# Optimization experiments

Measured on AMD Instinct MI355X. Metric: run time of the kernel, lower is better.

Reference implementation:

```python
import jax, jax.numpy as jnp
import numpy as np

B, T_ENC, IN, H, SEQ_OUT = 1024, 50, 99, 2112, 25


def _lstm_cell(x, h, c, W_ih, b_ih, W_hh, b_hh):
    # gates: [B, 4H], torch LSTMCell gate order is i, f, g, o
    gates = x @ W_ih.T + b_ih + h @ W_hh.T + b_hh
    i, f, g, o = jnp.split(gates, 4, axis=-1)
    c_new = jax.nn.sigmoid(f) * c + jax.nn.sigmoid(i) * jnp.tanh(g)
    h_new = jax.nn.sigmoid(o) * jnp.tanh(c_new)
    return h_new, c_new


def setup_inputs() -> dict:
    key = jax.random.key(0)
    ks = jax.random.split(key, 14)
    s = 0.04
    return {
        "hidden_states": jax.random.normal(ks[0], (B, T_ENC, H), jnp.float32),
        "cell_states": jax.random.normal(ks[1], (B, T_ENC, H), jnp.float32),
        "global_t_state": jax.random.normal(ks[2], (B, H), jnp.float32),
        "p": jax.random.normal(ks[3], (B, 1, IN), jnp.float32),
        "W_ih0": jax.random.normal(ks[4], (4 * H, IN), jnp.float32) * s,
        "b_ih0": jax.random.normal(ks[5], (4 * H,), jnp.float32) * s,
        "W_hh0": jax.random.normal(ks[6], (4 * H, H), jnp.float32) * s,
        "b_hh0": jax.random.normal(ks[7], (4 * H,), jnp.float32) * s,
        "W_ih1": jax.random.normal(ks[8], (4 * H, H), jnp.float32) * s,
        "b_ih1": jax.random.normal(ks[9], (4 * H,), jnp.float32) * s,
        "W_hh1": jax.random.normal(ks[10], (4 * H, H), jnp.float32) * s,
        "b_hh1": jax.random.normal(ks[11], (4 * H,), jnp.float32) * s,
        "W_out": jax.random.normal(ks[12], (H, IN), jnp.float32) * s,
        "b_out": jax.random.normal(ks[13], (IN,), jnp.float32) * s,
    }


def reference(hidden_states, cell_states, global_t_state, p,
              W_ih0, b_ih0, W_hh0, b_hh0,
              W_ih1, b_ih1, W_hh1, b_hh1,
              W_out, b_out):
    # initial states: layer 0 uses mean over encoder hidden states,
    # layer 1 uses mean over [global_t_state ; hidden_states]
    h0 = hidden_states.mean(axis=1)                                   # [B, H]
    h1 = jnp.concatenate((global_t_state[:, None, :], hidden_states), axis=1).mean(axis=1)
    c0 = cell_states.mean(axis=1)
    c1 = c0
    pre0 = p[:, 0, :]                                                 # seed input [B, IN]

    def step(carry, _):
        h0, c0, h1, c1, prev = carry
        h0n, c0n = _lstm_cell(prev, h0, c0, W_ih0, b_ih0, W_hh0, b_hh0)
        h1n, c1n = _lstm_cell(h0n, h1, c1, W_ih1, b_ih1, W_hh1, b_hh1)
        pre = h1n @ W_out + b_out + prev                              # residual on cell-0 input
        return (h0n, c0n, h1n, c1n, pre), pre

    _, pres = jax.lax.scan(step, (h0, c0, h1, c1, pre0), None, length=SEQ_OUT)
    return pres.transpose(1, 0, 2)                                    # [B, SEQ_OUT, IN]
```

## Files before the change

### kernel.cpp

```cpp
#include <hip/hip_runtime.h>

#define B_    1024
#define H_    2112
#define FH    8448
#define IN_   99
#define TENC  50
#define SEQ   25
#define K0    2240
#define K1    4224
#define LDX0  2240
#define LDX1  4224

typedef __bf16 bf16;
typedef __bf16 bf16x8 __attribute__((ext_vector_type(8)));
typedef __bf16 bf16x4 __attribute__((ext_vector_type(4)));
typedef float  f32x4  __attribute__((ext_vector_type(4)));

__device__ __forceinline__ void gload_lds16(const void* g, void* l) {
  __builtin_amdgcn_global_load_lds(
      (const __attribute__((address_space(1))) void*)g,
      (__attribute__((address_space(3))) void*)l, 16, 0, 0);
}

__device__ __forceinline__ float sigf(float x) { return 1.f / (1.f + __expf(-x)); }
__device__ __forceinline__ float tanhfast(float x) { return 1.f - 2.f / (__expf(2.f * x) + 1.f); }

__global__ __launch_bounds__(256, 2)
void lstm_gemm_cell(const bf16* __restrict__ X, int lda, int K,
                    const bf16* __restrict__ W,
                    const float* __restrict__ bsum,
                    float* __restrict__ Cst,
                    bf16* __restrict__ d1, int ld1,
                    bf16* __restrict__ d2, int ld2)
{
  __shared__ __align__(16) bf16 As0[128 * 32];
  __shared__ __align__(16) bf16 As1[128 * 32];
  __shared__ __align__(16) bf16 Bs0[128 * 32];
  __shared__ __align__(16) bf16 Bs1[128 * 32];

  const int vid = (blockIdx.x & 7) * 66 + (blockIdx.x >> 3);
  const int hb  = vid >> 3;
  const int hc0 = hb * 32;
  const int m0  = (vid & 7) * 128;

  const int tid  = threadIdx.x;
  const int srow = tid >> 2;
  const int scol = (tid & 3) * 8;

  const bf16* Ab = X + (size_t)(m0 + srow) * lda + scol;
  const bf16* Bb = W + ((size_t)((srow >> 5) * H_ + hc0 + (srow & 31))) * K + scol;
  const size_t HK2 = (size_t)2 * H_ * K;

  const int lane = tid & 63;
  const int wv = tid >> 6;
  const int wm = wv >> 1, wn = wv & 1;
  const int lr = lane & 15, lq = lane >> 4;

  f32x4 acc[4][4];
#pragma unroll
  for (int a = 0; a < 4; ++a)
#pragma unroll
    for (int b = 0; b < 4; ++b) acc[a][b] = (f32x4){0.f, 0.f, 0.f, 0.f};

#define STAGE(kt, AD, BD) do {                                              \
    const int ko_ = (kt) * 32;                                              \
    gload_lds16(Ab + (size_t)0 * lda + ko_,  &AD[0 * 2048 + tid * 8]);      \
    gload_lds16(Ab + (size_t)64 * lda + ko_, &AD[1 * 2048 + tid * 8]);      \
    gload_lds16(Bb + ko_,                    &BD[0 * 2048 + tid * 8]);      \
    gload_lds16(Bb + HK2 + ko_,              &BD[1 * 2048 + tid * 8]);      \
  } while (0)

#define COMPUTE(AS, BS) do {                                                \
    bf16x8 af_[4], bf_[4];                                                  \
    _Pragma("unroll")                                                       \
    for (int mi = 0; mi < 4; ++mi)                                          \
      af_[mi] = *(const bf16x8*)&AS[(wm * 64 + mi * 16 + lr) * 32 + lq * 8];\
    _Pragma("unroll")                                                       \
    for (int nf = 0; nf < 4; ++nf)                                          \
      bf_[nf] = *(const bf16x8*)&BS[(nf * 32 + wn * 16 + lr) * 32 + lq * 8];\
    _Pragma("unroll")                                                       \
    for (int mi = 0; mi < 4; ++mi)                                          \
      _Pragma("unroll")                                                     \
      for (int nf = 0; nf < 4; ++nf)                                        \
        acc[mi][nf] = __builtin_amdgcn_mfma_f32_16x16x32_bf16(              \
            af_[mi], bf_[nf], acc[mi][nf], 0, 0, 0);                        \
  } while (0)

  const int KT = K >> 5;
  STAGE(0, As0, Bs0);
  __syncthreads();
  for (int kt = 0; kt < KT; kt += 2) {
    STAGE(kt + 1, As1, Bs1);
    COMPUTE(As0, Bs0);
    __syncthreads();
    if (kt + 2 < KT) STAGE(kt + 2, As0, Bs0);
    COMPUTE(As1, Bs1);
    __syncthreads();
  }
#undef STAGE
#undef COMPUTE

  const int hc = hc0 + wn * 16 + lr;
  const float bi  = bsum[hc];
  const float bff = bsum[H_ + hc];
  const float bg  = bsum[2 * H_ + hc];
  const float bo  = bsum[3 * H_ + hc];

#pragma unroll
  for (int mi = 0; mi < 4; ++mi) {
#pragma unroll
    for (int r = 0; r < 4; ++r) {
      const int m = m0 + wm * 64 + mi * 16 + lq * 4 + r;
      const float gi = acc[mi][0][r] + bi;
      const float gf = acc[mi][1][r] + bff;
      const float gg = acc[mi][2][r] + bg;
      const float go = acc[mi][3][r] + bo;
      const size_t ci = (size_t)m * H_ + hc;
      const float c_old = Cst[ci];
      const float cn = sigf(gf) * c_old + sigf(gi) * tanhfast(gg);
      const float hn = sigf(go) * tanhfast(cn);
      Cst[ci] = cn;
      const bf16 hb2 = (bf16)hn;
      d1[(size_t)m * ld1 + hc] = hb2;
      if (d2) d2[(size_t)m * ld2 + hc] = hb2;
    }
  }
}

__global__ __launch_bounds__(256, 1)
void out_gemm(const bf16* __restrict__ Hin,
              const bf16* __restrict__ Wo,
              const float* __restrict__ b_out,
              float* __restrict__ prev,
              bf16* __restrict__ X0n,
              float* __restrict__ out, int t)
{
  __shared__ float red[4][4][112];
  const int tid = threadIdx.x;
  const int m0 = blockIdx.x * 4;
  const int lane = tid & 63, wv = tid >> 6;
  const int lr = lane & 15, lq = lane >> 4, lk = lq * 8;

  f32x4 acc[7];
#pragma unroll
  for (int b = 0; b < 7; ++b) acc[b] = (f32x4){0.f, 0.f, 0.f, 0.f};

  const int start = (wv == 0) ? 0 : (1 + wv * 8);
  const int cnt = (wv == 0) ? 9 : 8;

  for (int kt = start; kt < start + cnt; ++kt) {
    const int ko = kt * 64;
    bf16x8 av[2], bv[7][2];
#pragma unroll
    for (int kc = 0; kc < 2; ++kc)
      av[kc] = *(const bf16x8*)&Hin[(size_t)(m0 + (lr & 3)) * LDX1 + ko + kc * 32 + lk];
#pragma unroll
    for (int nf = 0; nf < 7; ++nf)
#pragma unroll
      for (int kc = 0; kc < 2; ++kc)
        bv[nf][kc] = *(const bf16x8*)&Wo[(size_t)(nf * 16 + lr) * H_ + ko + kc * 32 + lk];
#pragma unroll
    for (int nf = 0; nf < 7; ++nf)
#pragma unroll
      for (int kc = 0; kc < 2; ++kc)
        acc[nf] = __builtin_amdgcn_mfma_f32_16x16x32_bf16(av[kc], bv[nf][kc], acc[nf], 0, 0, 0);
  }

  if (lq == 0) {
#pragma unroll
    for (int nf = 0; nf < 7; ++nf)
#pragma unroll
      for (int r = 0; r < 4; ++r)
        red[wv][r][nf * 16 + lr] = acc[nf][r];
  }
  __syncthreads();

  for (int idx = tid; idx < 4 * 112; idx += 256) {
    const int ml = idx / 112, n = idx - ml * 112;
    if (n < IN_) {
      const int m = m0 + ml;
      float s = red[0][ml][n] + red[1][ml][n] + red[2][ml][n] + red[3][ml][n] + b_out[n];
      const float pre = s + prev[m * 112 + n];
      prev[m * 112 + n] = pre;
      out[((size_t)m * SEQ + t) * IN_ + n] = pre;
      X0n[(size_t)m * LDX0 + n] = (bf16)pre;
    }
  }
}

__global__ void init_state(const float* __restrict__ hs, const float* __restrict__ cs,
                           const float* __restrict__ gts,
                           bf16* __restrict__ X0a, bf16* __restrict__ X1a,
                           float* __restrict__ c0, float* __restrict__ c1)
{
  const int h4 = blockIdx.x * 256 + threadIdx.x;
  if (h4 >= 528) return;
  const int b = blockIdx.y;
  const float4* hp = (const float4*)(hs + (size_t)b * TENC * H_) + h4;
  const float4* cp = (const float4*)(cs + (size_t)b * TENC * H_) + h4;
  float4 sh = {0.f, 0.f, 0.f, 0.f}, sc = {0.f, 0.f, 0.f, 0.f};
  for (int tt = 0; tt < TENC; ++tt) {
    float4 a = hp[tt * 528];
    sh.x += a.x; sh.y += a.y; sh.z += a.z; sh.w += a.w;
    float4 c = cp[tt * 528];
    sc.x += c.x; sc.y += c.y; sc.z += c.z; sc.w += c.w;
  }
  const float4 g = ((const float4*)(gts + (size_t)b * H_))[h4];
  const float4 c0v = {sc.x / 50.f, sc.y / 50.f, sc.z / 50.f, sc.w / 50.f};
  ((float4*)(c0 + (size_t)b * H_))[h4] = c0v;
  ((float4*)(c1 + (size_t)b * H_))[h4] = c0v;
  bf16x4 h0b = {(bf16)(sh.x / 50.f), (bf16)(sh.y / 50.f), (bf16)(sh.z / 50.f), (bf16)(sh.w / 50.f)};
  *(bf16x4*)&X0a[(size_t)b * LDX0 + 128 + h4 * 4] = h0b;
  bf16x4 h1b = {(bf16)((sh.x + g.x) / 51.f), (bf16)((sh.y + g.y) / 51.f),
                (bf16)((sh.z + g.z) / 51.f), (bf16)((sh.w + g.w) / 51.f)};
  *(bf16x4*)&X1a[(size_t)b * LDX1 + 2112 + h4 * 4] = h1b;
}

__global__ void init_prev(const float* __restrict__ p, float* __restrict__ prev,
                          bf16* __restrict__ X0a, bf16* __restrict__ X0b)
{
  const int idx = blockIdx.x * 256 + threadIdx.x;
  const int b = idx >> 7, n = idx & 127;
  const float v = (n < IN_) ? p[(size_t)b * IN_ + n] : 0.f;
  if (n < 112) prev[b * 112 + n] = v;
  X0a[(size_t)b * LDX0 + n] = (bf16)v;
  X0b[(size_t)b * LDX0 + n] = (bf16)0.f;
}

__global__ void pack_w0(const float* __restrict__ Wih, const float* __restrict__ Whh,
                        bf16* __restrict__ Wc)
{
  const int n = blockIdx.x;
  const float* a = Wih + (size_t)n * IN_;
  const float* b = Whh + (size_t)n * H_;
  bf16* d = Wc + (size_t)n * K0;
  for (int k = threadIdx.x; k < K0; k += 256) {
    float v = (k < IN_) ? a[k] : ((k >= 128) ? b[k - 128] : 0.f);
    d[k] = (bf16)v;
  }
}

__global__ void pack_w1(const float* __restrict__ Wih, const float* __restrict__ Whh,
                        bf16* __restrict__ Wc)
{
  const int n = blockIdx.x;
  bf16* d = Wc + (size_t)n * K1;
  for (int k = threadIdx.x; k < K1; k += 256)
    d[k] = (bf16)((k < H_) ? Wih[(size_t)n * H_ + k] : Whh[(size_t)n * H_ + k - H_]);
}

__global__ void pack_wo(const float* __restrict__ W, bf16* __restrict__ Wo)
{
  const int n = blockIdx.x;
  for (int k = threadIdx.x; k < H_; k += 256)
    Wo[(size_t)n * H_ + k] = (n < IN_) ? (bf16)W[(size_t)k * IN_ + n] : (bf16)0.f;
}

__global__ void pack_bias(const float* __restrict__ bi0, const float* __restrict__ bh0,
                          const float* __restrict__ bi1, const float* __restrict__ bh1,
                          float* __restrict__ bs0, float* __restrict__ bs1)
{
  const int i = blockIdx.x * 256 + threadIdx.x;
  if (i < FH) { bs0[i] = bi0[i] + bh0[i]; bs1[i] = bi1[i] + bh1[i]; }
}

extern "C" void kernel_launch(void* const* d_in, const int* in_sizes, int n_in,
                              void* d_out, int out_size, void* d_ws, size_t ws_size,
                              hipStream_t stream)
{
  (void)in_sizes; (void)n_in; (void)out_size; (void)ws_size;
  const float* hs   = (const float*)d_in[0];
  const float* cs   = (const float*)d_in[1];
  const float* gts  = (const float*)d_in[2];
  const float* p    = (const float*)d_in[3];
  const float* Wih0 = (const float*)d_in[4];
  const float* bih0 = (const float*)d_in[5];
  const float* Whh0 = (const float*)d_in[6];
  const float* bhh0 = (const float*)d_in[7];
  const float* Wih1 = (const float*)d_in[8];
  const float* bih1 = (const float*)d_in[9];
  const float* Whh1 = (const float*)d_in[10];
  const float* bhh1 = (const float*)d_in[11];
  const float* Wout = (const float*)d_in[12];
  const float* bout = (const float*)d_in[13];
  float* out = (float*)d_out;

  char* ws = (char*)d_ws;
  size_t off = 0;
  auto alloc = [&](size_t bytes) -> void* {
    void* q = ws + off; off += (bytes + 255) & ~(size_t)255; return q;
  };
  bf16* Wc0 = (bf16*)alloc((size_t)FH * K0 * 2);
  bf16* Wc1 = (bf16*)alloc((size_t)FH * K1 * 2);
  bf16* Wo  = (bf16*)alloc((size_t)112 * H_ * 2);
  float* bs0 = (float*)alloc((size_t)FH * 4);
  float* bs1 = (float*)alloc((size_t)FH * 4);
  bf16* X0[2] = {(bf16*)alloc((size_t)B_ * LDX0 * 2), (bf16*)alloc((size_t)B_ * LDX0 * 2)};
  bf16* X1[2] = {(bf16*)alloc((size_t)B_ * LDX1 * 2), (bf16*)alloc((size_t)B_ * LDX1 * 2)};
  float* c0  = (float*)alloc((size_t)B_ * H_ * 4);
  float* c1  = (float*)alloc((size_t)B_ * H_ * 4);
  float* prev = (float*)alloc((size_t)B_ * 112 * 4);

  pack_w0<<<FH, 256, 0, stream>>>(Wih0, Whh0, Wc0);
  pack_w1<<<FH, 256, 0, stream>>>(Wih1, Whh1, Wc1);
  pack_wo<<<112, 256, 0, stream>>>(Wout, Wo);
  pack_bias<<<(FH + 255) / 256, 256, 0, stream>>>(bih0, bhh0, bih1, bhh1, bs0, bs1);
  init_prev<<<(B_ * 128) / 256, 256, 0, stream>>>(p, prev, X0[0], X0[1]);
  init_state<<<dim3(3, B_), 256, 0, stream>>>(hs, cs, gts, X0[0], X1[0], c0, c1);

  for (int t = 0; t < SEQ; ++t) {
    const int cur = t & 1, nxt = cur ^ 1;
    lstm_gemm_cell<<<528, 256, 0, stream>>>(
        X0[cur], LDX0, K0, Wc0, bs0, c0, X1[cur], LDX1, X0[nxt] + 128, LDX0);
    lstm_gemm_cell<<<528, 256, 0, stream>>>(
        X1[cur], LDX1, K1, Wc1, bs1, c1, X1[nxt] + 2112, LDX1, (bf16*)nullptr, 0);
    out_gemm<<<256, 256, 0, stream>>>(X1[nxt] + 2112, Wo, bout, prev, X0[nxt], out, t);
  }
}
```

Baseline: 4.666 ms.

## Deepen LSTM GEMM K-tile to 64 with XOR-swizzled LDS and explicit vmcnt pipelining

Doubles the K tile from 32 to 64 per stage, so each barrier round covers twice the MFMA work. It adds an XOR swizzle on the LDS column layout to avoid bank conflicts on the fragment reads. The main loop is rebuilt with explicit s_waitcnt vmcnt, raw barriers, sched_barrier and setprio, so the next stage's global-to-LDS loads are issued right after fragments are read and overlap with the MFMAs. LDS use doubles to 64KB per block, which may limit the two-blocks-per-CU occupancy, and the hand-placed waitcnt counts must match the load counts exactly.

```diff
diff --git a/kernel.cpp b/kernel.cpp
--- a/kernel.cpp
+++ b/kernel.cpp
@@ -33,10 +33,10 @@
                     bf16* __restrict__ d1, int ld1,
                     bf16* __restrict__ d2, int ld2)
 {
-  __shared__ __align__(16) bf16 As0[128 * 32];
-  __shared__ __align__(16) bf16 As1[128 * 32];
-  __shared__ __align__(16) bf16 Bs0[128 * 32];
-  __shared__ __align__(16) bf16 Bs1[128 * 32];
+  __shared__ __align__(16) bf16 As0[128 * 64];
+  __shared__ __align__(16) bf16 As1[128 * 64];
+  __shared__ __align__(16) bf16 Bs0[128 * 64];
+  __shared__ __align__(16) bf16 Bs1[128 * 64];
 
   const int vid = (blockIdx.x & 7) * 66 + (blockIdx.x >> 3);
   const int hb  = vid >> 3;
@@ -44,17 +44,20 @@
   const int m0  = (vid & 7) * 128;
 
   const int tid  = threadIdx.x;
-  const int srow = tid >> 2;
-  const int scol = (tid & 3) * 8;
+  const int srow = tid >> 3;
+  const int scol = ((tid & 7) ^ (srow & 7)) * 8;
 
   const bf16* Ab = X + (size_t)(m0 + srow) * lda + scol;
-  const bf16* Bb = W + ((size_t)((srow >> 5) * H_ + hc0 + (srow & 31))) * K + scol;
-  const size_t HK2 = (size_t)2 * H_ * K;
+  const bf16* Bb = W + (size_t)(hc0 + srow) * K + scol;
+  const size_t HK = (size_t)H_ * K;
 
   const int lane = tid & 63;
   const int wv = tid >> 6;
   const int wm = wv >> 1, wn = wv & 1;
   const int lr = lane & 15, lq = lane >> 4;
+  const int xs = lr & 7;
+  const int cof0 = (lq ^ xs) * 8;
+  const int cof1 = ((4 + lq) ^ xs) * 8;
 
   f32x4 acc[4][4];
 #pragma unroll
@@ -62,43 +65,64 @@
 #pragma unroll
     for (int b = 0; b < 4; ++b) acc[a][b] = (f32x4){0.f, 0.f, 0.f, 0.f};
 
-#define STAGE(kt, AD, BD) do {                                              \
-    const int ko_ = (kt) * 32;                                              \
-    gload_lds16(Ab + (size_t)0 * lda + ko_,  &AD[0 * 2048 + tid * 8]);      \
-    gload_lds16(Ab + (size_t)64 * lda + ko_, &AD[1 * 2048 + tid * 8]);      \
-    gload_lds16(Bb + ko_,                    &BD[0 * 2048 + tid * 8]);      \
-    gload_lds16(Bb + HK2 + ko_,              &BD[1 * 2048 + tid * 8]);      \
+#define STAGE(kt, AD, BD) do {                                               \
+    const int ko_ = (kt) * 64;                                               \
+    _Pragma("unroll")                                                        \
+    for (int it = 0; it < 4; ++it)                                           \
+      gload_lds16(Ab + (size_t)(it * 32) * lda + ko_, &AD[it * 2048 + tid * 8]); \
+    _Pragma("unroll")                                                        \
+    for (int it = 0; it < 4; ++it)                                           \
+      gload_lds16(Bb + (size_t)it * HK + ko_, &BD[it * 2048 + tid * 8]);     \
   } while (0)
 
-#define COMPUTE(AS, BS) do {                                                \
-    bf16x8 af_[4], bf_[4];                                                  \
-    _Pragma("unroll")                                                       \
-    for (int mi = 0; mi < 4; ++mi)                                          \
-      af_[mi] = *(const bf16x8*)&AS[(wm * 64 + mi * 16 + lr) * 32 + lq * 8];\
-    _Pragma("unroll")                                                       \
-    for (int nf = 0; nf < 4; ++nf)                                          \
-      bf_[nf] = *(const bf16x8*)&BS[(nf * 32 + wn * 16 + lr) * 32 + lq * 8];\
-    _Pragma("unroll")                                                       \
-    for (int mi = 0; mi < 4; ++mi)                                          \
-      _Pragma("unroll")                                                     \
-      for (int nf = 0; nf < 4; ++nf)                                        \
-        acc[mi][nf] = __builtin_amdgcn_mfma_f32_16x16x32_bf16(              \
-            af_[mi], bf_[nf], acc[mi][nf], 0, 0, 0);                        \
+#define HALF(AS, BS, V8, DOSTAGE, kt2) do {                                  \
+    if (V8) asm volatile("s_waitcnt vmcnt(8)" ::: "memory");                 \
+    else    asm volatile("s_waitcnt vmcnt(0)" ::: "memory");                 \
+    __builtin_amdgcn_s_barrier();                                            \
+    __builtin_amdgcn_sched_barrier(0);                                       \
+    bf16x8 af_[4][2], bf_[4][2];                                             \
+    _Pragma("unroll")                                                        \
+    for (int mi = 0; mi < 4; ++mi) {                                         \
+      const int r_ = (wm * 64 + mi * 16 + lr) * 64;                          \
+      af_[mi][0] = *(const bf16x8*)&AS[r_ + cof0];                           \
+      af_[mi][1] = *(const bf16x8*)&AS[r_ + cof1];                           \
+    }                                                                        \
+    _Pragma("unroll")                                                        \
+    for (int nf = 0; nf < 4; ++nf) {                                         \
+      const int r_ = (nf * 32 + wn * 16 + lr) * 64;                          \
+      bf_[nf][0] = *(const bf16x8*)&BS[r_ + cof0];                           \
+      bf_[nf][1] = *(const bf16x8*)&BS[r_ + cof1];                           \
+    }                                                                        \
+    asm volatile("s_waitcnt lgkmcnt(0)" ::: "memory");                       \
+    __builtin_amdgcn_s_barrier();                                            \
+    __builtin_amdgcn_sched_barrier(0);                                       \
+    if (DOSTAGE) STAGE(kt2, AS, BS);                                         \
+    __builtin_amdgcn_s_setprio(1);                                           \
+    _Pragma("unroll")                                                        \
+    for (int kc = 0; kc < 2; ++kc)                                           \
+      _Pragma("unroll")                                                      \
+      for (int mi = 0; mi < 4; ++mi)                                         \
+        _Pragma("unroll")                                                    \
+        for (int nf = 0; nf < 4; ++nf)                                       \
+          acc[mi][nf] = __builtin_amdgcn_mfma_f32_16x16x32_bf16(             \
+              af_[mi][kc], bf_[nf][kc], acc[mi][nf], 0, 0, 0);               \
+    __builtin_amdgcn_s_setprio(0);                                           \
   } while (0)
 
-  const int KT = K >> 5;
+  const int KT = K >> 6;
   STAGE(0, As0, Bs0);
-  __syncthreads();
-  for (int kt = 0; kt < KT; kt += 2) {
-    STAGE(kt + 1, As1, Bs1);
-    COMPUTE(As0, Bs0);
-    __syncthreads();
-    if (kt + 2 < KT) STAGE(kt + 2, As0, Bs0);
-    COMPUTE(As1, Bs1);
-    __syncthreads();
-  }
+  STAGE(1, As1, Bs1);
+
+  int kt = 0;
+  for (; kt + 2 <= KT; kt += 2) {
+    HALF(As0, Bs0, true, (kt + 2 < KT), kt + 2);
+    HALF(As1, Bs1, (kt + 2 < KT), (kt + 3 < KT), kt + 3);
+  }
+  if (KT & 1) {
+    HALF(As0, Bs0, false, false, 0);
+  }
+#undef HALF
 #undef STAGE
-#undef COMPUTE
 
   const int hc = hc0 + wn * 16 + lr;
   const float bi  = bsum[hc];
```

New measurement: 5.245 ms. 1.12x slower.

## Split K across wave pairs in LSTM GEMM with LDS reduction

Applied to the files above, without the earlier changes.

Changes the LSTM gate GEMM so each wave covers the full 128-column N tile, and the two wave pairs alternate K slices (even and odd stages) instead of splitting N. The partial accumulators are then reduced through LDS in two rounds before the cell epilogue, which only the ks==0 waves run. The aim is more B-fragment reuse per A load per wave and fewer LDS reads per MFMA. In exchange it doubles accumulator registers to 128 floats per lane, which risks occupancy at launch bounds (256,2), and adds extra syncs plus an LDS reduction.

```diff
diff --git a/kernel.cpp b/kernel.cpp
--- a/kernel.cpp
+++ b/kernel.cpp
@@ -33,10 +33,11 @@
                     bf16* __restrict__ d1, int ld1,
                     bf16* __restrict__ d2, int ld2)
 {
-  __shared__ __align__(16) bf16 As0[128 * 32];
-  __shared__ __align__(16) bf16 As1[128 * 32];
-  __shared__ __align__(16) bf16 Bs0[128 * 32];
-  __shared__ __align__(16) bf16 Bs1[128 * 32];
+  __shared__ __align__(16) bf16 S[4 * 4096];
+  bf16* const As0 = S;
+  bf16* const As1 = S + 4096;
+  bf16* const Bs0 = S + 8192;
+  bf16* const Bs1 = S + 12288;
 
   const int vid = (blockIdx.x & 7) * 66 + (blockIdx.x >> 3);
   const int hb  = vid >> 3;
@@ -48,42 +49,42 @@
   const int scol = (tid & 3) * 8;
 
   const bf16* Ab = X + (size_t)(m0 + srow) * lda + scol;
-  const bf16* Bb = W + ((size_t)((srow >> 5) * H_ + hc0 + (srow & 31))) * K + scol;
+  const bf16* Bb = W + ((size_t)(srow >> 5) * H_ + hc0 + (srow & 31)) * K + scol;
   const size_t HK2 = (size_t)2 * H_ * K;
 
   const int lane = tid & 63;
   const int wv = tid >> 6;
-  const int wm = wv >> 1, wn = wv & 1;
+  const int wm = wv >> 1, ks = wv & 1;
   const int lr = lane & 15, lq = lane >> 4;
 
-  f32x4 acc[4][4];
+  f32x4 acc[4][8];
 #pragma unroll
   for (int a = 0; a < 4; ++a)
 #pragma unroll
-    for (int b = 0; b < 4; ++b) acc[a][b] = (f32x4){0.f, 0.f, 0.f, 0.f};
-
-#define STAGE(kt, AD, BD) do {                                              \
-    const int ko_ = (kt) * 32;                                              \
-    gload_lds16(Ab + (size_t)0 * lda + ko_,  &AD[0 * 2048 + tid * 8]);      \
-    gload_lds16(Ab + (size_t)64 * lda + ko_, &AD[1 * 2048 + tid * 8]);      \
-    gload_lds16(Bb + ko_,                    &BD[0 * 2048 + tid * 8]);      \
-    gload_lds16(Bb + HK2 + ko_,              &BD[1 * 2048 + tid * 8]);      \
+    for (int b = 0; b < 8; ++b) acc[a][b] = (f32x4){0.f, 0.f, 0.f, 0.f};
+
+#define STAGE(kt, AD, BD) do {                                               \
+    const int ko_ = (kt) * 32;                                               \
+    gload_lds16(Ab + ko_,                    &AD[tid * 8]);                  \
+    gload_lds16(Ab + (size_t)64 * lda + ko_, &AD[2048 + tid * 8]);           \
+    gload_lds16(Bb + ko_,                    &BD[tid * 8]);                  \
+    gload_lds16(Bb + HK2 + ko_,              &BD[2048 + tid * 8]);           \
   } while (0)
 
-#define COMPUTE(AS, BS) do {                                                \
-    bf16x8 af_[4], bf_[4];                                                  \
-    _Pragma("unroll")                                                       \
-    for (int mi = 0; mi < 4; ++mi)                                          \
-      af_[mi] = *(const bf16x8*)&AS[(wm * 64 + mi * 16 + lr) * 32 + lq * 8];\
-    _Pragma("unroll")                                                       \
-    for (int nf = 0; nf < 4; ++nf)                                          \
-      bf_[nf] = *(const bf16x8*)&BS[(nf * 32 + wn * 16 + lr) * 32 + lq * 8];\
-    _Pragma("unroll")                                                       \
-    for (int mi = 0; mi < 4; ++mi)                                          \
-      _Pragma("unroll")                                                     \
-      for (int nf = 0; nf < 4; ++nf)                                        \
-        acc[mi][nf] = __builtin_amdgcn_mfma_f32_16x16x32_bf16(              \
-            af_[mi], bf_[nf], acc[mi][nf], 0, 0, 0);                        \
+#define COMPUTE(AS, BS) do {                                                 \
+    bf16x8 af_[4], bf_[8];                                                   \
+    _Pragma("unroll")                                                        \
+    for (int mi = 0; mi < 4; ++mi)                                           \
+      af_[mi] = *(const bf16x8*)&AS[(wm * 64 + mi * 16 + lr) * 32 + lq * 8]; \
+    _Pragma("unroll")                                                        \
+    for (int nf = 0; nf < 8; ++nf)                                           \
+      bf_[nf] = *(const bf16x8*)&BS[(nf * 16 + lr) * 32 + lq * 8];           \
+    _Pragma("unroll")                                                        \
+    for (int mi = 0; mi < 4; ++mi)                                           \
+      _Pragma("unroll")                                                      \
+      for (int nf = 0; nf < 8; ++nf)                                         \
+        acc[mi][nf] = __builtin_amdgcn_mfma_f32_16x16x32_bf16(               \
+            af_[mi], bf_[nf], acc[mi][nf], 0, 0, 0);                         \
   } while (0)
 
   const int KT = K >> 5;
@@ -91,38 +92,63 @@
   __syncthreads();
   for (int kt = 0; kt < KT; kt += 2) {
     STAGE(kt + 1, As1, Bs1);
-    COMPUTE(As0, Bs0);
+    if (ks == 0) COMPUTE(As0, Bs0);
     __syncthreads();
     if (kt + 2 < KT) STAGE(kt + 2, As0, Bs0);
-    COMPUTE(As1, Bs1);
+    if (ks == 1) COMPUTE(As1, Bs1);
     __syncthreads();
   }
+#undef COMPUTE
 #undef STAGE
-#undef COMPUTE
-
-  const int hc = hc0 + wn * 16 + lr;
-  const float bi  = bsum[hc];
-  const float bff = bsum[H_ + hc];
-  const float bg  = bsum[2 * H_ + hc];
-  const float bo  = bsum[3 * H_ + hc];
-
-#pragma unroll
-  for (int mi = 0; mi < 4; ++mi) {
-#pragma unroll
-    for (int r = 0; r < 4; ++r) {
-      const int m = m0 + wm * 64 + mi * 16 + lq * 4 + r;
-      const float gi = acc[mi][0][r] + bi;
-      const float gf = acc[mi][1][r] + bff;
-      const float gg = acc[mi][2][r] + bg;
-      const float go = acc[mi][3][r] + bo;
-      const size_t ci = (size_t)m * H_ + hc;
-      const float c_old = Cst[ci];
-      const float cn = sigf(gf) * c_old + sigf(gi) * tanhfast(gg);
-      const float hn = sigf(go) * tanhfast(cn);
-      Cst[ci] = cn;
-      const bf16 hb2 = (bf16)hn;
-      d1[(size_t)m * ld1 + hc] = hb2;
-      if (d2) d2[(size_t)m * ld2 + hc] = hb2;
+
+  f32x4* red = (f32x4*)S;
+#pragma unroll
+  for (int round = 0; round < 2; ++round) {
+    if (wm == round && ks == 1) {
+#pragma unroll
+      for (int mi = 0; mi < 4; ++mi)
+#pragma unroll
+        for (int nf = 0; nf < 8; ++nf)
+          red[(mi * 8 + nf) * 64 + lane] = acc[mi][nf];
+    }
+    __syncthreads();
+    if (wm == round && ks == 0) {
+#pragma unroll
+      for (int mi = 0; mi < 4; ++mi)
+#pragma unroll
+        for (int nf = 0; nf < 8; ++nf)
+          acc[mi][nf] += red[(mi * 8 + nf) * 64 + lane];
+    }
+    __syncthreads();
+  }
+
+  if (ks != 0) return;
+
+#pragma unroll
+  for (int hh = 0; hh < 2; ++hh) {
+    const int hc = hc0 + hh * 16 + lr;
+    const float bi  = bsum[hc];
+    const float bff = bsum[H_ + hc];
+    const float bg  = bsum[2 * H_ + hc];
+    const float bo  = bsum[3 * H_ + hc];
+#pragma unroll
+    for (int mi = 0; mi < 4; ++mi) {
+#pragma unroll
+      for (int r = 0; r < 4; ++r) {
+        const int m = m0 + wm * 64 + mi * 16 + lq * 4 + r;
+        const float gi = acc[mi][0 + hh][r] + bi;
+        const float gf = acc[mi][2 + hh][r] + bff;
+        const float gg = acc[mi][4 + hh][r] + bg;
+        const float go = acc[mi][6 + hh][r] + bo;
+        const size_t ci = (size_t)m * H_ + hc;
+        const float c_old = Cst[ci];
+        const float cn = sigf(gf) * c_old + sigf(gi) * tanhfast(gg);
+        const float hn = sigf(go) * tanhfast(cn);
+        Cst[ci] = cn;
+        const bf16 hb2 = (bf16)hn;
+        d1[(size_t)m * ld1 + hc] = hb2;
+        if (d2) d2[(size_t)m * ld2 + hc] = hb2;
+      }
     }
   }
 }
```

New measurement: 6.772 ms. 1.45x slower.
